# Kernel tuning notes

Hardware: AMD Instinct MI355X
Metric: run time of the kernel (lower is better)

The kernel has to match this reference:

```python
import jax, jax.numpy as jnp
import numpy as np

B, N, D, H, QK, HID = 4, 1024, 1024, 16, 64, 4096
BETA = 1.0 / float(np.sqrt(QK))  # default attn_beta = 1/sqrt(qk_dim)


def setup_inputs() -> dict:
    key = jax.random.key(0)
    k1, k2, k3, k4 = jax.random.split(key, 4)
    x = jax.random.normal(k1, (B, N, D), dtype=jnp.float32)
    scale = 1.0 / float(np.sqrt(D))
    Wq = jax.random.normal(k2, (H, QK, D), dtype=jnp.float32) * scale
    Wk = jax.random.normal(k3, (H, QK, D), dtype=jnp.float32) * scale
    W_hop = jax.random.normal(k4, (D, HID), dtype=jnp.float32) * scale
    return {"x": x, "Wq": Wq, "Wk": Wk, "W_hop": W_hop}


def _energy(x, Wq, Wk, W_hop):
    # Graph energy attention (dense path, no adjacency / mask)
    q = jnp.einsum('bnd,hqd->bhnq', x, Wq)  # [B,H,N,QK]
    k = jnp.einsum('bnd,hqd->bhnq', x, Wk)  # [B,H,N,QK]
    scores = BETA * jnp.einsum('bhnq,bhmq->bhnm', q, k)  # [B,H,N,N]
    e_attn = -(1.0 / BETA) * jnp.sum(jax.nn.logsumexp(scores, axis=-1))
    # Hopfield energy: -1/2 * sum relu(x W)^2
    h = jax.nn.relu(jnp.einsum('bnd,de->bne', x, W_hop))  # [B,N,HID]
    e_hop = -0.5 * jnp.sum(h * h)
    return e_attn + e_hop


def reference(x, Wq, Wk, W_hop):
    # Module returns (grad of energy w.r.t. x, energy) via grad_and_value
    energy, grad = jax.value_and_grad(_energy, argnums=0)(x, Wq, Wk, W_hop)
    return grad, energy
```

## Files before the change

kernel.cpp:

```cpp
#include <hip/hip_runtime.h>
#include <hip/hip_bf16.h>
#include <math.h>

#define BETA 0.125f
#define INV_BETA 8.0f

typedef __attribute__((ext_vector_type(8))) short short8v;
typedef __attribute__((ext_vector_type(4))) float f32x4;
typedef union { short8v v; unsigned short u[8]; } v8u;

#define OFF_XB   0u
#define OFF_WCB  2097152u
#define OFF_WCTB 3145728u
#define OFF_WHB  4194304u
#define OFF_WHTB 6291456u
#define OFF_H    8388608u
#define OFF_QB   16777216u
#define OFF_KB   18874368u
#define OFF_QT   20971520u
#define OFF_KT   23068672u
#define OFF_DQK  25165824u
#define OFF_LSE  29360128u
#define OFF_PL   29425664u
#define OFF_PH   29427712u

__device__ __forceinline__ unsigned short f2b(float f) {
    unsigned u = __float_as_uint(f);
    return (unsigned short)((u + 0x7fffu + ((u >> 16) & 1u)) >> 16);
}

__device__ __forceinline__ void gload_lds16(const unsigned short* g, void* l) {
    __builtin_amdgcn_global_load_lds(
        (const __attribute__((address_space(1))) unsigned int*)g,
        (__attribute__((address_space(3))) unsigned int*)l, 16, 0, 0);
}

__global__ __launch_bounds__(256) void k_cast(const float* __restrict__ src,
                                              unsigned short* __restrict__ dst, int n4) {
    int i = blockIdx.x * 256 + threadIdx.x;
    if (i < n4) {
        float4 v = ((const float4*)src)[i];
        ushort4 o;
        o.x = f2b(v.x); o.y = f2b(v.y); o.z = f2b(v.z); o.w = f2b(v.w);
        ((ushort4*)dst)[i] = o;
    }
}

__global__ void k_tcatb(const float* __restrict__ Wq, const float* __restrict__ Wk,
                        unsigned short* __restrict__ WCTB) {
    __shared__ float t[32][33];
    int j0 = blockIdx.x * 32, d0 = blockIdx.y * 32;
    int tx = threadIdx.x, ty = threadIdx.y;
#pragma unroll
    for (int i = 0; i < 4; ++i) {
        int j = j0 + ty + 8 * i;
        const float* src = (j < 1024) ? (Wq + (size_t)j * 1024) : (Wk + (size_t)(j - 1024) * 1024);
        t[ty + 8 * i][tx] = src[d0 + tx];
    }
    __syncthreads();
#pragma unroll
    for (int i = 0; i < 4; ++i)
        WCTB[(size_t)(d0 + ty + 8 * i) * 2048 + j0 + tx] = f2b(t[tx][ty + 8 * i]);
}

__global__ void k_thopb(const float* __restrict__ Whop, unsigned short* __restrict__ WHTB) {
    __shared__ float t[32][33];
    int e0 = blockIdx.x * 32, d0 = blockIdx.y * 32;
    int tx = threadIdx.x, ty = threadIdx.y;
#pragma unroll
    for (int i = 0; i < 4; ++i)
        t[ty + 8 * i][tx] = Whop[(size_t)(d0 + ty + 8 * i) * 4096 + e0 + tx];
    __syncthreads();
#pragma unroll
    for (int i = 0; i < 4; ++i)
        WHTB[(size_t)(e0 + ty + 8 * i) * 1024 + d0 + tx] = f2b(t[tx][ty + 8 * i]);
}

template <int NJ>
__device__ __forceinline__ void gemm_core(const unsigned short* __restrict__ A, int lda,
                                          const unsigned short* __restrict__ Bm, int ldb,
                                          int kdim, int rowBase, int colBase,
                                          unsigned short* ldsA, unsigned short* ldsB,
                                          f32x4 (&acc)[4][NJ]) {
    const int tid = threadIdx.x, lane = tid & 63;
    const int wv = tid >> 6;
    const int lr = lane & 15, lg = lane >> 4;
    const int wrow = (wv >> 1) * 64;
    const int wcol = (wv & 1) * (NJ * 16);

    for (int kk = 0; kk < kdim; kk += 64) {
#pragma unroll
        for (int iss = 0; iss < 4; ++iss) {
            int p = iss * 256 + tid;
            int row = p >> 3, c = p & 7, cs = c ^ (row & 7);
            gload_lds16(&A[(size_t)(rowBase + row) * lda + kk + cs * 8], (char*)ldsA + p * 16);
        }
#pragma unroll
        for (int iss = 0; iss < NJ; ++iss) {
            int p = iss * 256 + tid;
            int row = p >> 3, c = p & 7, cs = c ^ (row & 7);
            gload_lds16(&Bm[(size_t)(colBase + row) * ldb + kk + cs * 8], (char*)ldsB + p * 16);
        }
        __syncthreads();
#pragma unroll
        for (int kc = 0; kc < 2; ++kc) {
            short8v av[4], bv[NJ];
#pragma unroll
            for (int i = 0; i < 4; ++i) {
                int row = wrow + i * 16 + lr;
                int phys = row * 128 + ((kc * 4 + lg) ^ (row & 7)) * 16;
                av[i] = *(const short8v*)((const char*)ldsA + phys);
            }
#pragma unroll
            for (int j = 0; j < NJ; ++j) {
                int row = wcol + j * 16 + lr;
                int phys = row * 128 + ((kc * 4 + lg) ^ (row & 7)) * 16;
                bv[j] = *(const short8v*)((const char*)ldsB + phys);
            }
#pragma unroll
            for (int i = 0; i < 4; ++i)
#pragma unroll
                for (int j = 0; j < NJ; ++j)
                    acc[i][j] = __builtin_amdgcn_mfma_f32_16x16x32_bf16(av[i], bv[j], acc[i][j], 0, 0, 0);
        }
        __syncthreads();
    }
}

#define GEMM_SETUP(NJ)                                                           \
    __shared__ unsigned short ldsA[128 * 64];                                    \
    __shared__ unsigned short ldsB[NJ * 32 * 64];                                \
    const int tid = threadIdx.x, lane = tid & 63, wv = tid >> 6;                 \
    const int lr = lane & 15, lg = lane >> 4;                                    \
    const int row0 = blockIdx.x * 128 + (wv >> 1) * 64;                          \
    const int col0 = blockIdx.y * (NJ * 32) + (wv & 1) * (NJ * 16);              \
    f32x4 acc[4][NJ];                                                            \
    _Pragma("unroll") for (int i = 0; i < 4; ++i)                                \
        _Pragma("unroll") for (int j = 0; j < NJ; ++j)                           \
            acc[i][j] = (f32x4){0.f, 0.f, 0.f, 0.f};

__global__ __launch_bounds__(256) void mm_proj(const unsigned short* __restrict__ XB,
                                               const unsigned short* __restrict__ WCB,
                                               unsigned short* __restrict__ Qb,
                                               unsigned short* __restrict__ Kb) {
    GEMM_SETUP(4)
    gemm_core<4>(XB, 1024, WCB, 1024, 1024, blockIdx.x * 128, blockIdx.y * 128, ldsA, ldsB, acc);
    unsigned short* dst = (col0 < 1024) ? Qb : Kb;
    const int cbase = col0 & 1023;
#pragma unroll
    for (int i = 0; i < 4; ++i)
#pragma unroll
        for (int r = 0; r < 4; ++r) {
            int rg = row0 + i * 16 + lg * 4 + r;
            int bb = rg >> 10, n = rg & 1023;
#pragma unroll
            for (int j = 0; j < 4; ++j) {
                int c = cbase + j * 16 + lr;
                int h = c >> 6, q = c & 63;
                dst[((size_t)(bb * 16 + h) * 1024 + n) * 64 + q] = f2b(acc[i][j][r]);
            }
        }
}

__global__ __launch_bounds__(256) void mm_hopfwd(const unsigned short* __restrict__ XB,
                                                 const unsigned short* __restrict__ WHTB,
                                                 unsigned short* __restrict__ H,
                                                 float* __restrict__ PH) {
    __shared__ float red[4];
    GEMM_SETUP(4)
    gemm_core<4>(XB, 1024, WHTB, 1024, 1024, blockIdx.x * 128, blockIdx.y * 128, ldsA, ldsB, acc);
    float ss = 0.f;
#pragma unroll
    for (int i = 0; i < 4; ++i)
#pragma unroll
        for (int r = 0; r < 4; ++r) {
            size_t rg = row0 + i * 16 + lg * 4 + r;
#pragma unroll
            for (int j = 0; j < 4; ++j) {
                float hv = fmaxf(acc[i][j][r], 0.f);
                ss += hv * hv;
                H[rg * 4096 + col0 + j * 16 + lr] = f2b(hv);
            }
        }
#pragma unroll
    for (int off = 32; off; off >>= 1) ss += __shfl_down(ss, off);
    if (lane == 0) red[wv] = ss;
    __syncthreads();
    if (tid == 0) PH[blockIdx.y * gridDim.x + blockIdx.x] = red[0] + red[1] + red[2] + red[3];
}

__global__ __launch_bounds__(256) void mm_hopbwd(const unsigned short* __restrict__ H,
                                                 const unsigned short* __restrict__ WHB,
                                                 float* __restrict__ out) {
    GEMM_SETUP(2)
    gemm_core<2>(H, 4096, WHB, 4096, 4096, blockIdx.x * 128, blockIdx.y * 64, ldsA, ldsB, acc);
#pragma unroll
    for (int i = 0; i < 4; ++i)
#pragma unroll
        for (int r = 0; r < 4; ++r) {
            size_t rg = row0 + i * 16 + lg * 4 + r;
#pragma unroll
            for (int j = 0; j < 2; ++j)
                out[rg * 1024 + col0 + j * 16 + lr] = -acc[i][j][r];
        }
}

__global__ __launch_bounds__(256) void mm_gradproj(const unsigned short* __restrict__ DQK,
                                                   const unsigned short* __restrict__ WCTB,
                                                   float* __restrict__ out) {
    GEMM_SETUP(2)
    gemm_core<2>(DQK, 2048, WCTB, 2048, 2048, blockIdx.x * 128, blockIdx.y * 64, ldsA, ldsB, acc);
#pragma unroll
    for (int i = 0; i < 4; ++i)
#pragma unroll
        for (int r = 0; r < 4; ++r) {
            size_t rg = row0 + i * 16 + lg * 4 + r;
#pragma unroll
            for (int j = 0; j < 2; ++j) {
                size_t idx = rg * 1024 + col0 + j * 16 + lr;
                out[idx] += acc[i][j][r];
            }
        }
}

__global__ __launch_bounds__(256) void k_tqk(const unsigned short* __restrict__ Qb,
                                             const unsigned short* __restrict__ Kb,
                                             unsigned short* __restrict__ QT,
                                             unsigned short* __restrict__ KT) {
    __shared__ unsigned short T[64][65];
    const int z = blockIdx.z;
    const unsigned short* src = z ? Kb : Qb;
    unsigned short* dst = z ? KT : QT;
    const int bh = blockIdx.y;
    const int n0 = blockIdx.x * 64;
    const int t = threadIdx.x;
    {
        int row = t >> 3;
        int colc = (t & 7) * 8;
#pragma unroll
        for (int ii = 0; ii < 2; ++ii) {
            int r = row + 32 * ii;
            v8u vv;
            vv.v = *(const short8v*)&src[((size_t)(bh << 10) + n0 + r) * 64 + colc];
#pragma unroll
            for (int j = 0; j < 8; ++j) T[r][colc + j] = vv.u[j];
        }
    }
    __syncthreads();
    {
        int q = t >> 2;
        int nc = (t & 3) * 16;
        unsigned short buf[16];
#pragma unroll
        for (int j = 0; j < 16; ++j) buf[j] = T[nc + j][q];
        *(short8v*)&dst[((size_t)bh * 64 + q) * 1024 + n0 + nc] = *(short8v*)&buf[0];
        *(short8v*)&dst[((size_t)bh * 64 + q) * 1024 + n0 + nc + 8] = *(short8v*)&buf[8];
    }
}

__global__ __launch_bounds__(256) void k_dq(const unsigned short* __restrict__ Qb,
                                            const unsigned short* __restrict__ Kb,
                                            const unsigned short* __restrict__ KT,
                                            float* __restrict__ LSE,
                                            float* __restrict__ PL,
                                            unsigned short* __restrict__ DQK) {
    __shared__ unsigned short Ktile[2][64 * 64];
    __shared__ unsigned short Ttile[2][64 * 64];
    __shared__ unsigned short P[4][2048];
    const int tid = threadIdx.x, lane = tid & 63, wv = tid >> 6;
    const int bh = blockIdx.x, nt = blockIdx.y;
    const int nw = nt * 128 + wv * 32;
    const int lr = lane & 15, lg = lane >> 4;
    unsigned short* Pw = &P[wv][0];

    auto stage = [&](int buf, int m0) {
#pragma unroll
        for (int iss = 0; iss < 2; ++iss) {
            int p = iss * 256 + tid;
            int row = p >> 3, c = p & 7, cs = c ^ (row & 7);
            gload_lds16(&Kb[((size_t)(bh << 10) + m0 + row) * 64 + cs * 8],
                        (char*)&Ktile[buf][0] + p * 16);
            gload_lds16(&KT[((size_t)bh * 64 + row) * 1024 + m0 + cs * 8],
                        (char*)&Ttile[buf][0] + p * 16);
        }
    };

    short8v qa[2][2];
#pragma unroll
    for (int rb = 0; rb < 2; ++rb)
#pragma unroll
        for (int kc = 0; kc < 2; ++kc)
            qa[rb][kc] = *(const short8v*)&Qb[((size_t)(bh << 10) + nw + rb * 16 + lr) * 64 + kc * 32 + lg * 8];

    float sm[2][4];
    f32x4 dq[2][4];
#pragma unroll
    for (int rb = 0; rb < 2; ++rb) {
#pragma unroll
        for (int r = 0; r < 4; ++r) sm[rb][r] = 0.f;
#pragma unroll
        for (int qb = 0; qb < 4; ++qb) dq[rb][qb] = (f32x4){0.f, 0.f, 0.f, 0.f};
    }

    stage(0, 0);
    __syncthreads();
    int buf = 0;
    for (int mt = 0; mt < 16; ++mt) {
        if (mt < 15) stage(buf ^ 1, (mt + 1) * 64);
        const char* Kt = (const char*)&Ktile[buf][0];
        const char* Tt = (const char*)&Ttile[buf][0];
#pragma unroll
        for (int ct = 0; ct < 4; ++ct) {
            int brow = ct * 16 + lr;
            short8v bk0 = *(const short8v*)(Kt + brow * 128 + ((lg) ^ (brow & 7)) * 16);
            short8v bk1 = *(const short8v*)(Kt + brow * 128 + ((lg + 4) ^ (brow & 7)) * 16);
#pragma unroll
            for (int rb = 0; rb < 2; ++rb) {
                f32x4 s = {0.f, 0.f, 0.f, 0.f};
                s = __builtin_amdgcn_mfma_f32_16x16x32_bf16(qa[rb][0], bk0, s, 0, 0, 0);
                s = __builtin_amdgcn_mfma_f32_16x16x32_bf16(qa[rb][1], bk1, s, 0, 0, 0);
#pragma unroll
                for (int r = 0; r < 4; ++r) {
                    float p = __expf(s[r] * BETA);
                    sm[rb][r] += p;
                    int row = rb * 16 + lg * 4 + r;
                    int off = (row * 64 + ct * 16 + lr) ^ ((row & 7) << 3);
                    Pw[off] = f2b(p);
                }
            }
        }
        short8v pa[2][2];
#pragma unroll
        for (int rb = 0; rb < 2; ++rb) {
            int row = rb * 16 + lr;
#pragma unroll
            for (int kc = 0; kc < 2; ++kc) {
                int off = (row * 64 + kc * 32 + lg * 8) ^ ((row & 7) << 3);
                pa[rb][kc] = *(const short8v*)&Pw[off];
            }
        }
#pragma unroll
        for (int qb = 0; qb < 4; ++qb) {
            int brow = qb * 16 + lr;
            short8v b0 = *(const short8v*)(Tt + brow * 128 + ((lg) ^ (brow & 7)) * 16);
            short8v b1 = *(const short8v*)(Tt + brow * 128 + ((lg + 4) ^ (brow & 7)) * 16);
#pragma unroll
            for (int rb = 0; rb < 2; ++rb) {
                dq[rb][qb] = __builtin_amdgcn_mfma_f32_16x16x32_bf16(pa[rb][0], b0, dq[rb][qb], 0, 0, 0);
                dq[rb][qb] = __builtin_amdgcn_mfma_f32_16x16x32_bf16(pa[rb][1], b1, dq[rb][qb], 0, 0, 0);
            }
        }
        __syncthreads();
        buf ^= 1;
    }

#pragma unroll
    for (int off = 1; off < 16; off <<= 1)
#pragma unroll
        for (int rb = 0; rb < 2; ++rb)
#pragma unroll
            for (int r = 0; r < 4; ++r) sm[rb][r] += __shfl_xor(sm[rb][r], off);

    const int b = bh >> 4, h = bh & 15;
#pragma unroll
    for (int rb = 0; rb < 2; ++rb) {
#pragma unroll
        for (int r = 0; r < 4; ++r) {
            float inv = 1.0f / sm[rb][r];
#pragma unroll
            for (int qb = 0; qb < 4; ++qb)
                DQK[((size_t)(b << 10) + nw + rb * 16 + lg * 4 + r) * 2048 + h * 64 + qb * 16 + lr] =
                    f2b(-dq[rb][qb][r] * inv);
        }
    }

    float lsum = 0.f;
    if (lr == 0) {
#pragma unroll
        for (int rb = 0; rb < 2; ++rb)
#pragma unroll
            for (int r = 0; r < 4; ++r) {
                float l = __logf(sm[rb][r]);
                LSE[(size_t)(bh << 10) + nw + rb * 16 + lg * 4 + r] = l;
                lsum += l;
            }
    }
    lsum += __shfl_xor(lsum, 16);
    lsum += __shfl_xor(lsum, 32);
    if (lane == 0) PL[(size_t)(bh * 8 + nt) * 4 + wv] = lsum;
}

__global__ __launch_bounds__(256) void k_dk(const unsigned short* __restrict__ Qb,
                                            const unsigned short* __restrict__ Kb,
                                            const unsigned short* __restrict__ QT,
                                            const float* __restrict__ LSE,
                                            unsigned short* __restrict__ DQK) {
    __shared__ unsigned short Qtile[2][64 * 64];
    __shared__ unsigned short Ttile[2][64 * 64];
    __shared__ unsigned short P[4][2048];
    const int tid = threadIdx.x, lane = tid & 63, wv = tid >> 6;
    const int bh = blockIdx.x, mt = blockIdx.y;
    const int mw = mt * 128 + wv * 32;
    const int lr = lane & 15, lg = lane >> 4;
    unsigned short* Pw = &P[wv][0];

    auto stage = [&](int buf, int n0) {
#pragma unroll
        for (int iss = 0; iss < 2; ++iss) {
            int p = iss * 256 + tid;
            int row = p >> 3, c = p & 7, cs = c ^ (row & 7);
            gload_lds16(&Qb[((size_t)(bh << 10) + n0 + row) * 64 + cs * 8],
                        (char*)&Qtile[buf][0] + p * 16);
            gload_lds16(&QT[((size_t)bh * 64 + row) * 1024 + n0 + cs * 8],
                        (char*)&Ttile[buf][0] + p * 16);
        }
    };

    short8v ka[2][2];
#pragma unroll
    for (int rb = 0; rb < 2; ++rb)
#pragma unroll
        for (int kc = 0; kc < 2; ++kc)
            ka[rb][kc] = *(const short8v*)&Kb[((size_t)(bh << 10) + mw + rb * 16 + lr) * 64 + kc * 32 + lg * 8];

    f32x4 dk[2][4];
#pragma unroll
    for (int rb = 0; rb < 2; ++rb)
#pragma unroll
        for (int qb = 0; qb < 4; ++qb) dk[rb][qb] = (f32x4){0.f, 0.f, 0.f, 0.f};

    stage(0, 0);
    __syncthreads();
    int buf = 0;
    for (int ntl = 0; ntl < 16; ++ntl) {
        const int n0 = ntl * 64;
        float lse_c[4];
#pragma unroll
        for (int ct = 0; ct < 4; ++ct)
            lse_c[ct] = LSE[(size_t)(bh << 10) + n0 + ct * 16 + lr];
        if (ntl < 15) stage(buf ^ 1, n0 + 64);
        const char* Qt = (const char*)&Qtile[buf][0];
        const char* Tt = (const char*)&Ttile[buf][0];
#pragma unroll
        for (int ct = 0; ct < 4; ++ct) {
            int brow = ct * 16 + lr;
            short8v bq0 = *(const short8v*)(Qt + brow * 128 + ((lg) ^ (brow & 7)) * 16);
            short8v bq1 = *(const short8v*)(Qt + brow * 128 + ((lg + 4) ^ (brow & 7)) * 16);
#pragma unroll
            for (int rb = 0; rb < 2; ++rb) {
                f32x4 s = {0.f, 0.f, 0.f, 0.f};
                s = __builtin_amdgcn_mfma_f32_16x16x32_bf16(ka[rb][0], bq0, s, 0, 0, 0);
                s = __builtin_amdgcn_mfma_f32_16x16x32_bf16(ka[rb][1], bq1, s, 0, 0, 0);
#pragma unroll
                for (int r = 0; r < 4; ++r) {
                    float p = __expf(s[r] * BETA - lse_c[ct]);
                    int row = rb * 16 + lg * 4 + r;
                    int off = (row * 64 + ct * 16 + lr) ^ ((row & 7) << 3);
                    Pw[off] = f2b(p);
                }
            }
        }
        short8v pa[2][2];
#pragma unroll
        for (int rb = 0; rb < 2; ++rb) {
            int row = rb * 16 + lr;
#pragma unroll
            for (int kc = 0; kc < 2; ++kc) {
                int off = (row * 64 + kc * 32 + lg * 8) ^ ((row & 7) << 3);
                pa[rb][kc] = *(const short8v*)&Pw[off];
            }
        }
#pragma unroll
        for (int qb = 0; qb < 4; ++qb) {
            int brow = qb * 16 + lr;
            short8v b0 = *(const short8v*)(Tt + brow * 128 + ((lg) ^ (brow & 7)) * 16);
            short8v b1 = *(const short8v*)(Tt + brow * 128 + ((lg + 4) ^ (brow & 7)) * 16);
#pragma unroll
            for (int rb = 0; rb < 2; ++rb) {
                dk[rb][qb] = __builtin_amdgcn_mfma_f32_16x16x32_bf16(pa[rb][0], b0, dk[rb][qb], 0, 0, 0);
                dk[rb][qb] = __builtin_amdgcn_mfma_f32_16x16x32_bf16(pa[rb][1], b1, dk[rb][qb], 0, 0, 0);
            }
        }
        __syncthreads();
        buf ^= 1;
    }
    const int b = bh >> 4, h = bh & 15;
#pragma unroll
    for (int rb = 0; rb < 2; ++rb)
#pragma unroll
        for (int qb = 0; qb < 4; ++qb)
#pragma unroll
            for (int r = 0; r < 4; ++r)
                DQK[((size_t)(b << 10) + mw + rb * 16 + lg * 4 + r) * 2048 + 1024 + h * 64 + qb * 16 + lr] = f2b(-dk[rb][qb][r]);
}

__global__ __launch_bounds__(256) void k_fin(const float* __restrict__ pl,
                                             const float* __restrict__ ph,
                                             float* __restrict__ out) {
    const int tid = threadIdx.x;
    float s1 = 0.f, s2 = 0.f;
    for (int i = tid; i < 2048; i += 256) s1 += pl[i];
    for (int i = tid; i < 1024; i += 256) s2 += ph[i];
#pragma unroll
    for (int off = 32; off; off >>= 1) {
        s1 += __shfl_down(s1, off);
        s2 += __shfl_down(s2, off);
    }
    __shared__ float r1[4], r2[4];
    if ((tid & 63) == 0) { r1[tid >> 6] = s1; r2[tid >> 6] = s2; }
    __syncthreads();
    if (tid == 0) {
        float S1 = r1[0] + r1[1] + r1[2] + r1[3];
        float S2 = r2[0] + r2[1] + r2[2] + r2[3];
        out[(size_t)4194304] = -INV_BETA * S1 - 0.5f * S2;
    }
}

extern "C" void kernel_launch(void* const* d_in, const int* in_sizes, int n_in,
                              void* d_out, int out_size, void* d_ws, size_t ws_size,
                              hipStream_t stream) {
    (void)in_sizes; (void)n_in; (void)out_size; (void)ws_size;
    const float* x    = (const float*)d_in[0];
    const float* Wq   = (const float*)d_in[1];
    const float* Wk   = (const float*)d_in[2];
    const float* Whop = (const float*)d_in[3];
    float* out = (float*)d_out;
    float* ws = (float*)d_ws;

    unsigned short* XB   = (unsigned short*)(ws + OFF_XB);
    unsigned short* WCB  = (unsigned short*)(ws + OFF_WCB);
    unsigned short* WCTB = (unsigned short*)(ws + OFF_WCTB);
    unsigned short* WHB  = (unsigned short*)(ws + OFF_WHB);
    unsigned short* WHTB = (unsigned short*)(ws + OFF_WHTB);
    unsigned short* H    = (unsigned short*)(ws + OFF_H);
    unsigned short* Qb   = (unsigned short*)(ws + OFF_QB);
    unsigned short* Kb   = (unsigned short*)(ws + OFF_KB);
    unsigned short* QT   = (unsigned short*)(ws + OFF_QT);
    unsigned short* KT   = (unsigned short*)(ws + OFF_KT);
    unsigned short* DQK  = (unsigned short*)(ws + OFF_DQK);
    float* LSE = ws + OFF_LSE;
    float* PL  = ws + OFF_PL;
    float* PH  = ws + OFF_PH;

    dim3 blk(256);
    k_cast<<<dim3(4096), blk, 0, stream>>>(x, XB, 1048576);
    k_cast<<<dim3(1024), blk, 0, stream>>>(Wq, WCB, 262144);
    k_cast<<<dim3(1024), blk, 0, stream>>>(Wk, WCB + 1048576, 262144);
    k_cast<<<dim3(4096), blk, 0, stream>>>(Whop, WHB, 1048576);
    k_tcatb<<<dim3(64, 32), dim3(32, 8), 0, stream>>>(Wq, Wk, WCTB);
    k_thopb<<<dim3(128, 32), dim3(32, 8), 0, stream>>>(Whop, WHTB);

    mm_proj<<<dim3(32, 16), blk, 0, stream>>>(XB, WCB, Qb, Kb);
    k_tqk<<<dim3(16, 64, 2), blk, 0, stream>>>(Qb, Kb, QT, KT);
    k_dq<<<dim3(64, 8), blk, 0, stream>>>(Qb, Kb, KT, LSE, PL, DQK);
    k_dk<<<dim3(64, 8), blk, 0, stream>>>(Qb, Kb, QT, LSE, DQK);

    mm_hopfwd<<<dim3(32, 32), blk, 0, stream>>>(XB, WHTB, H, PH);
    mm_hopbwd<<<dim3(32, 16), blk, 0, stream>>>(H, WHB, out);
    mm_gradproj<<<dim3(32, 16), blk, 0, stream>>>(DQK, WCTB, out);
    k_fin<<<dim3(1), blk, 0, stream>>>(PL, PH, out);
}
```

Before: 328.0 us.

## Double-buffer LDS in GEMM cores and merge cast/transpose launches

Adds a double-buffered GEMM core that prefetches the next K tile into a second LDS buffer while MFMAs run on the current one, and uses it for the projection, Hopfield backward and gradient-projection GEMMs. The four cast kernels are merged into one launch, and the two transpose kernels into one, to cut launch overhead. Double buffering doubles LDS use per block, which may lower occupancy.

```diff
diff --git a/kernel.cpp b/kernel.cpp
--- a/kernel.cpp
+++ b/kernel.cpp
@@ -35,45 +35,55 @@
         (__attribute__((address_space(3))) unsigned int*)l, 16, 0, 0);
 }
 
-__global__ __launch_bounds__(256) void k_cast(const float* __restrict__ src,
-                                              unsigned short* __restrict__ dst, int n4) {
+__global__ __launch_bounds__(256) void k_castall(const float* __restrict__ x,
+                                                 const float* __restrict__ Wq,
+                                                 const float* __restrict__ Wk,
+                                                 const float* __restrict__ Whop,
+                                                 unsigned short* __restrict__ XB,
+                                                 unsigned short* __restrict__ WCB,
+                                                 unsigned short* __restrict__ WHB) {
     int i = blockIdx.x * 256 + threadIdx.x;
-    if (i < n4) {
-        float4 v = ((const float4*)src)[i];
-        ushort4 o;
-        o.x = f2b(v.x); o.y = f2b(v.y); o.z = f2b(v.z); o.w = f2b(v.w);
-        ((ushort4*)dst)[i] = o;
-    }
-}
-
-__global__ void k_tcatb(const float* __restrict__ Wq, const float* __restrict__ Wk,
-                        unsigned short* __restrict__ WCTB) {
+    const float* s;
+    unsigned short* d;
+    int j;
+    if (i < 1048576) { s = x; d = XB; j = i; }
+    else if (i < 1310720) { s = Wq; d = WCB; j = i - 1048576; }
+    else if (i < 1572864) { s = Wk; d = WCB + 1048576; j = i - 1310720; }
+    else { s = Whop; d = WHB; j = i - 1572864; }
+    float4 v = ((const float4*)s)[j];
+    ushort4 o;
+    o.x = f2b(v.x); o.y = f2b(v.y); o.z = f2b(v.z); o.w = f2b(v.w);
+    ((ushort4*)d)[j] = o;
+}
+
+__global__ void k_tall(const float* __restrict__ Wq, const float* __restrict__ Wk,
+                       const float* __restrict__ Whop,
+                       unsigned short* __restrict__ WCTB, unsigned short* __restrict__ WHTB) {
     __shared__ float t[32][33];
-    int j0 = blockIdx.x * 32, d0 = blockIdx.y * 32;
+    int bx = blockIdx.x;
     int tx = threadIdx.x, ty = threadIdx.y;
-#pragma unroll
-    for (int i = 0; i < 4; ++i) {
-        int j = j0 + ty + 8 * i;
-        const float* src = (j < 1024) ? (Wq + (size_t)j * 1024) : (Wk + (size_t)(j - 1024) * 1024);
-        t[ty + 8 * i][tx] = src[d0 + tx];
-    }
-    __syncthreads();
-#pragma unroll
-    for (int i = 0; i < 4; ++i)
-        WCTB[(size_t)(d0 + ty + 8 * i) * 2048 + j0 + tx] = f2b(t[tx][ty + 8 * i]);
-}
-
-__global__ void k_thopb(const float* __restrict__ Whop, unsigned short* __restrict__ WHTB) {
-    __shared__ float t[32][33];
-    int e0 = blockIdx.x * 32, d0 = blockIdx.y * 32;
-    int tx = threadIdx.x, ty = threadIdx.y;
-#pragma unroll
-    for (int i = 0; i < 4; ++i)
-        t[ty + 8 * i][tx] = Whop[(size_t)(d0 + ty + 8 * i) * 4096 + e0 + tx];
-    __syncthreads();
-#pragma unroll
-    for (int i = 0; i < 4; ++i)
-        WHTB[(size_t)(e0 + ty + 8 * i) * 1024 + d0 + tx] = f2b(t[tx][ty + 8 * i]);
+    if (bx < 64) {
+        int j0 = bx * 32, d0 = blockIdx.y * 32;
+#pragma unroll
+        for (int i = 0; i < 4; ++i) {
+            int j = j0 + ty + 8 * i;
+            const float* src = (j < 1024) ? (Wq + (size_t)j * 1024) : (Wk + (size_t)(j - 1024) * 1024);
+            t[ty + 8 * i][tx] = src[d0 + tx];
+        }
+        __syncthreads();
+#pragma unroll
+        for (int i = 0; i < 4; ++i)
+            WCTB[(size_t)(d0 + ty + 8 * i) * 2048 + j0 + tx] = f2b(t[tx][ty + 8 * i]);
+    } else {
+        int e0 = (bx - 64) * 32, d0 = blockIdx.y * 32;
+#pragma unroll
+        for (int i = 0; i < 4; ++i)
+            t[ty + 8 * i][tx] = Whop[(size_t)(d0 + ty + 8 * i) * 4096 + e0 + tx];
+        __syncthreads();
+#pragma unroll
+        for (int i = 0; i < 4; ++i)
+            WHTB[(size_t)(e0 + ty + 8 * i) * 1024 + d0 + tx] = f2b(t[tx][ty + 8 * i]);
+    }
 }
 
 template <int NJ>
@@ -127,9 +137,66 @@
     }
 }
 
-#define GEMM_SETUP(NJ)                                                           \
-    __shared__ unsigned short ldsA[128 * 64];                                    \
-    __shared__ unsigned short ldsB[NJ * 32 * 64];                                \
+template <int NJ>
+__device__ __forceinline__ void gemm_core_db(const unsigned short* __restrict__ A, int lda,
+                                             const unsigned short* __restrict__ Bm, int ldb,
+                                             int kdim, int rowBase, int colBase,
+                                             unsigned short (*ldsA)[128 * 64],
+                                             unsigned short (*ldsB)[NJ * 32 * 64],
+                                             f32x4 (&acc)[4][NJ]) {
+    const int tid = threadIdx.x, lane = tid & 63;
+    const int wv = tid >> 6;
+    const int lr = lane & 15, lg = lane >> 4;
+    const int wrow = (wv >> 1) * 64;
+    const int wcol = (wv & 1) * (NJ * 16);
+
+    auto stage = [&](int buf, int kk) {
+#pragma unroll
+        for (int iss = 0; iss < 4; ++iss) {
+            int p = iss * 256 + tid;
+            int row = p >> 3, c = p & 7, cs = c ^ (row & 7);
+            gload_lds16(&A[(size_t)(rowBase + row) * lda + kk + cs * 8], (char*)&ldsA[buf][0] + p * 16);
+        }
+#pragma unroll
+        for (int iss = 0; iss < NJ; ++iss) {
+            int p = iss * 256 + tid;
+            int row = p >> 3, c = p & 7, cs = c ^ (row & 7);
+            gload_lds16(&Bm[(size_t)(colBase + row) * ldb + kk + cs * 8], (char*)&ldsB[buf][0] + p * 16);
+        }
+    };
+
+    stage(0, 0);
+    __syncthreads();
+    int buf = 0;
+    for (int kk = 0; kk < kdim; kk += 64) {
+        if (kk + 64 < kdim) stage(buf ^ 1, kk + 64);
+        const char* La = (const char*)&ldsA[buf][0];
+        const char* Lb = (const char*)&ldsB[buf][0];
+#pragma unroll
+        for (int kc = 0; kc < 2; ++kc) {
+            short8v av[4], bv[NJ];
+#pragma unroll
+            for (int i = 0; i < 4; ++i) {
+                int row = wrow + i * 16 + lr;
+                av[i] = *(const short8v*)(La + row * 128 + ((kc * 4 + lg) ^ (row & 7)) * 16);
+            }
+#pragma unroll
+            for (int j = 0; j < NJ; ++j) {
+                int row = wcol + j * 16 + lr;
+                bv[j] = *(const short8v*)(Lb + row * 128 + ((kc * 4 + lg) ^ (row & 7)) * 16);
+            }
+#pragma unroll
+            for (int i = 0; i < 4; ++i)
+#pragma unroll
+                for (int j = 0; j < NJ; ++j)
+                    acc[i][j] = __builtin_amdgcn_mfma_f32_16x16x32_bf16(av[i], bv[j], acc[i][j], 0, 0, 0);
+        }
+        __syncthreads();
+        buf ^= 1;
+    }
+}
+
+#define GEMM_IDX(NJ)                                                             \
     const int tid = threadIdx.x, lane = tid & 63, wv = tid >> 6;                 \
     const int lr = lane & 15, lg = lane >> 4;                                    \
     const int row0 = blockIdx.x * 128 + (wv >> 1) * 64;                          \
@@ -143,8 +210,10 @@
                                                const unsigned short* __restrict__ WCB,
                                                unsigned short* __restrict__ Qb,
                                                unsigned short* __restrict__ Kb) {
-    GEMM_SETUP(4)
-    gemm_core<4>(XB, 1024, WCB, 1024, 1024, blockIdx.x * 128, blockIdx.y * 128, ldsA, ldsB, acc);
+    __shared__ unsigned short ldsA[2][128 * 64];
+    __shared__ unsigned short ldsB[2][128 * 64];
+    GEMM_IDX(4)
+    gemm_core_db<4>(XB, 1024, WCB, 1024, 1024, blockIdx.x * 128, blockIdx.y * 128, ldsA, ldsB, acc);
     unsigned short* dst = (col0 < 1024) ? Qb : Kb;
     const int cbase = col0 & 1023;
 #pragma unroll
@@ -166,8 +235,10 @@
                                                  const unsigned short* __restrict__ WHTB,
                                                  unsigned short* __restrict__ H,
                                                  float* __restrict__ PH) {
+    __shared__ unsigned short ldsA[128 * 64];
+    __shared__ unsigned short ldsB[128 * 64];
     __shared__ float red[4];
-    GEMM_SETUP(4)
+    GEMM_IDX(4)
     gemm_core<4>(XB, 1024, WHTB, 1024, 1024, blockIdx.x * 128, blockIdx.y * 128, ldsA, ldsB, acc);
     float ss = 0.f;
 #pragma unroll
@@ -192,8 +263,10 @@
 __global__ __launch_bounds__(256) void mm_hopbwd(const unsigned short* __restrict__ H,
                                                  const unsigned short* __restrict__ WHB,
                                                  float* __restrict__ out) {
-    GEMM_SETUP(2)
-    gemm_core<2>(H, 4096, WHB, 4096, 4096, blockIdx.x * 128, blockIdx.y * 64, ldsA, ldsB, acc);
+    __shared__ unsigned short ldsA[2][128 * 64];
+    __shared__ unsigned short ldsB[2][64 * 64];
+    GEMM_IDX(2)
+    gemm_core_db<2>(H, 4096, WHB, 4096, 4096, blockIdx.x * 128, blockIdx.y * 64, ldsA, ldsB, acc);
 #pragma unroll
     for (int i = 0; i < 4; ++i)
 #pragma unroll
@@ -208,8 +281,10 @@
 __global__ __launch_bounds__(256) void mm_gradproj(const unsigned short* __restrict__ DQK,
                                                    const unsigned short* __restrict__ WCTB,
                                                    float* __restrict__ out) {
-    GEMM_SETUP(2)
-    gemm_core<2>(DQK, 2048, WCTB, 2048, 2048, blockIdx.x * 128, blockIdx.y * 64, ldsA, ldsB, acc);
+    __shared__ unsigned short ldsA[2][128 * 64];
+    __shared__ unsigned short ldsB[2][64 * 64];
+    GEMM_IDX(2)
+    gemm_core_db<2>(DQK, 2048, WCTB, 2048, 2048, blockIdx.x * 128, blockIdx.y * 64, ldsA, ldsB, acc);
 #pragma unroll
     for (int i = 0; i < 4; ++i)
 #pragma unroll
@@ -543,12 +618,8 @@
     float* PH  = ws + OFF_PH;
 
     dim3 blk(256);
-    k_cast<<<dim3(4096), blk, 0, stream>>>(x, XB, 1048576);
-    k_cast<<<dim3(1024), blk, 0, stream>>>(Wq, WCB, 262144);
-    k_cast<<<dim3(1024), blk, 0, stream>>>(Wk, WCB + 1048576, 262144);
-    k_cast<<<dim3(4096), blk, 0, stream>>>(Whop, WHB, 1048576);
-    k_tcatb<<<dim3(64, 32), dim3(32, 8), 0, stream>>>(Wq, Wk, WCTB);
-    k_thopb<<<dim3(128, 32), dim3(32, 8), 0, stream>>>(Whop, WHTB);
+    k_castall<<<dim3(10240), blk, 0, stream>>>(x, Wq, Wk, Whop, XB, WCB, WHB);
+    k_tall<<<dim3(192, 32), dim3(32, 8), 0, stream>>>(Wq, Wk, Whop, WCTB, WHTB);
 
     mm_proj<<<dim3(32, 16), blk, 0, stream>>>(XB, WCB, Qb, Kb);
     k_tqk<<<dim3(16, 64, 2), blk, 0, stream>>>(Qb, Kb, QT, KT);
```

New measurement: 329.2 us. About the same (+0.4%).

## Shrink GEMM and attention tiles for more blocks; merge cast/transpose launches

Applied to the files above, without the earlier changes.

Templates the GEMM core on the row-tile count and halves the row tile for the projection, hop-backward and grad-projection GEMMs. This doubles their grid to 1024 blocks on a 256-CU device. The dq/dk attention kernels drop from 32 rows per wave to 16, which doubles their block count, and the partial-LSE buffer and final reduction grow to match. The six cast/transpose launches are merged into two kernels to cut launch overhead. The cost is less data reuse per block and more total loads of the shared operands.

```diff
diff --git a/kernel.cpp b/kernel.cpp
--- a/kernel.cpp
+++ b/kernel.cpp
@@ -22,7 +22,7 @@
 #define OFF_DQK  25165824u
 #define OFF_LSE  29360128u
 #define OFF_PL   29425664u
-#define OFF_PH   29427712u
+#define OFF_PH   29429760u
 
 __device__ __forceinline__ unsigned short f2b(float f) {
     unsigned u = __float_as_uint(f);
@@ -35,62 +35,72 @@
         (__attribute__((address_space(3))) unsigned int*)l, 16, 0, 0);
 }
 
-__global__ __launch_bounds__(256) void k_cast(const float* __restrict__ src,
-                                              unsigned short* __restrict__ dst, int n4) {
+__global__ __launch_bounds__(256) void k_castall(const float* __restrict__ x,
+                                                 const float* __restrict__ Wq,
+                                                 const float* __restrict__ Wk,
+                                                 const float* __restrict__ Whop,
+                                                 unsigned short* __restrict__ XB,
+                                                 unsigned short* __restrict__ WCB,
+                                                 unsigned short* __restrict__ WHB) {
     int i = blockIdx.x * 256 + threadIdx.x;
-    if (i < n4) {
-        float4 v = ((const float4*)src)[i];
-        ushort4 o;
-        o.x = f2b(v.x); o.y = f2b(v.y); o.z = f2b(v.z); o.w = f2b(v.w);
-        ((ushort4*)dst)[i] = o;
-    }
-}
-
-__global__ void k_tcatb(const float* __restrict__ Wq, const float* __restrict__ Wk,
-                        unsigned short* __restrict__ WCTB) {
+    const float* s;
+    unsigned short* d;
+    int j;
+    if (i < 1048576) { s = x; d = XB; j = i; }
+    else if (i < 1310720) { s = Wq; d = WCB; j = i - 1048576; }
+    else if (i < 1572864) { s = Wk; d = WCB + 1048576; j = i - 1310720; }
+    else { s = Whop; d = WHB; j = i - 1572864; }
+    float4 v = ((const float4*)s)[j];
+    ushort4 o;
+    o.x = f2b(v.x); o.y = f2b(v.y); o.z = f2b(v.z); o.w = f2b(v.w);
+    ((ushort4*)d)[j] = o;
+}
+
+__global__ void k_tall(const float* __restrict__ Wq, const float* __restrict__ Wk,
+                       const float* __restrict__ Whop,
+                       unsigned short* __restrict__ WCTB, unsigned short* __restrict__ WHTB) {
     __shared__ float t[32][33];
-    int j0 = blockIdx.x * 32, d0 = blockIdx.y * 32;
+    int bx = blockIdx.x;
     int tx = threadIdx.x, ty = threadIdx.y;
-#pragma unroll
-    for (int i = 0; i < 4; ++i) {
-        int j = j0 + ty + 8 * i;
-        const float* src = (j < 1024) ? (Wq + (size_t)j * 1024) : (Wk + (size_t)(j - 1024) * 1024);
-        t[ty + 8 * i][tx] = src[d0 + tx];
-    }
-    __syncthreads();
-#pragma unroll
-    for (int i = 0; i < 4; ++i)
-        WCTB[(size_t)(d0 + ty + 8 * i) * 2048 + j0 + tx] = f2b(t[tx][ty + 8 * i]);
-}
-
-__global__ void k_thopb(const float* __restrict__ Whop, unsigned short* __restrict__ WHTB) {
-    __shared__ float t[32][33];
-    int e0 = blockIdx.x * 32, d0 = blockIdx.y * 32;
-    int tx = threadIdx.x, ty = threadIdx.y;
-#pragma unroll
-    for (int i = 0; i < 4; ++i)
-        t[ty + 8 * i][tx] = Whop[(size_t)(d0 + ty + 8 * i) * 4096 + e0 + tx];
-    __syncthreads();
-#pragma unroll
-    for (int i = 0; i < 4; ++i)
-        WHTB[(size_t)(e0 + ty + 8 * i) * 1024 + d0 + tx] = f2b(t[tx][ty + 8 * i]);
-}
-
-template <int NJ>
+    if (bx < 64) {
+        int j0 = bx * 32, d0 = blockIdx.y * 32;
+#pragma unroll
+        for (int i = 0; i < 4; ++i) {
+            int j = j0 + ty + 8 * i;
+            const float* src = (j < 1024) ? (Wq + (size_t)j * 1024) : (Wk + (size_t)(j - 1024) * 1024);
+            t[ty + 8 * i][tx] = src[d0 + tx];
+        }
+        __syncthreads();
+#pragma unroll
+        for (int i = 0; i < 4; ++i)
+            WCTB[(size_t)(d0 + ty + 8 * i) * 2048 + j0 + tx] = f2b(t[tx][ty + 8 * i]);
+    } else {
+        int e0 = (bx - 64) * 32, d0 = blockIdx.y * 32;
+#pragma unroll
+        for (int i = 0; i < 4; ++i)
+            t[ty + 8 * i][tx] = Whop[(size_t)(d0 + ty + 8 * i) * 4096 + e0 + tx];
+        __syncthreads();
+#pragma unroll
+        for (int i = 0; i < 4; ++i)
+            WHTB[(size_t)(e0 + ty + 8 * i) * 1024 + d0 + tx] = f2b(t[tx][ty + 8 * i]);
+    }
+}
+
+template <int MI, int NJ>
 __device__ __forceinline__ void gemm_core(const unsigned short* __restrict__ A, int lda,
                                           const unsigned short* __restrict__ Bm, int ldb,
                                           int kdim, int rowBase, int colBase,
                                           unsigned short* ldsA, unsigned short* ldsB,
-                                          f32x4 (&acc)[4][NJ]) {
+                                          f32x4 (&acc)[MI][NJ]) {
     const int tid = threadIdx.x, lane = tid & 63;
     const int wv = tid >> 6;
     const int lr = lane & 15, lg = lane >> 4;
-    const int wrow = (wv >> 1) * 64;
+    const int wrow = (wv >> 1) * (MI * 16);
     const int wcol = (wv & 1) * (NJ * 16);
 
     for (int kk = 0; kk < kdim; kk += 64) {
 #pragma unroll
-        for (int iss = 0; iss < 4; ++iss) {
+        for (int iss = 0; iss < MI; ++iss) {
             int p = iss * 256 + tid;
             int row = p >> 3, c = p & 7, cs = c ^ (row & 7);
             gload_lds16(&A[(size_t)(rowBase + row) * lda + kk + cs * 8], (char*)ldsA + p * 16);
@@ -104,21 +114,19 @@
         __syncthreads();
 #pragma unroll
         for (int kc = 0; kc < 2; ++kc) {
-            short8v av[4], bv[NJ];
-#pragma unroll
-            for (int i = 0; i < 4; ++i) {
+            short8v av[MI], bv[NJ];
+#pragma unroll
+            for (int i = 0; i < MI; ++i) {
                 int row = wrow + i * 16 + lr;
-                int phys = row * 128 + ((kc * 4 + lg) ^ (row & 7)) * 16;
-                av[i] = *(const short8v*)((const char*)ldsA + phys);
+                av[i] = *(const short8v*)((const char*)ldsA + row * 128 + ((kc * 4 + lg) ^ (row & 7)) * 16);
             }
 #pragma unroll
             for (int j = 0; j < NJ; ++j) {
                 int row = wcol + j * 16 + lr;
-                int phys = row * 128 + ((kc * 4 + lg) ^ (row & 7)) * 16;
-                bv[j] = *(const short8v*)((const char*)ldsB + phys);
-            }
-#pragma unroll
-            for (int i = 0; i < 4; ++i)
+                bv[j] = *(const short8v*)((const char*)ldsB + row * 128 + ((kc * 4 + lg) ^ (row & 7)) * 16);
+            }
+#pragma unroll
+            for (int i = 0; i < MI; ++i)
 #pragma unroll
                 for (int j = 0; j < NJ; ++j)
                     acc[i][j] = __builtin_amdgcn_mfma_f32_16x16x32_bf16(av[i], bv[j], acc[i][j], 0, 0, 0);
@@ -127,15 +135,13 @@
     }
 }
 
-#define GEMM_SETUP(NJ)                                                           \
-    __shared__ unsigned short ldsA[128 * 64];                                    \
-    __shared__ unsigned short ldsB[NJ * 32 * 64];                                \
+#define GEMM_IDX(MI, NJ)                                                         \
     const int tid = threadIdx.x, lane = tid & 63, wv = tid >> 6;                 \
     const int lr = lane & 15, lg = lane >> 4;                                    \
-    const int row0 = blockIdx.x * 128 + (wv >> 1) * 64;                          \
+    const int row0 = blockIdx.x * (MI * 32) + (wv >> 1) * (MI * 16);             \
     const int col0 = blockIdx.y * (NJ * 32) + (wv & 1) * (NJ * 16);              \
-    f32x4 acc[4][NJ];                                                            \
-    _Pragma("unroll") for (int i = 0; i < 4; ++i)                                \
+    f32x4 acc[MI][NJ];                                                           \
+    _Pragma("unroll") for (int i = 0; i < MI; ++i)                               \
         _Pragma("unroll") for (int j = 0; j < NJ; ++j)                           \
             acc[i][j] = (f32x4){0.f, 0.f, 0.f, 0.f};
 
@@ -143,12 +149,14 @@
                                                const unsigned short* __restrict__ WCB,
                                                unsigned short* __restrict__ Qb,
                                                unsigned short* __restrict__ Kb) {
-    GEMM_SETUP(4)
-    gemm_core<4>(XB, 1024, WCB, 1024, 1024, blockIdx.x * 128, blockIdx.y * 128, ldsA, ldsB, acc);
+    __shared__ unsigned short ldsA[64 * 64];
+    __shared__ unsigned short ldsB[128 * 64];
+    GEMM_IDX(2, 4)
+    gemm_core<2, 4>(XB, 1024, WCB, 1024, 1024, blockIdx.x * 64, blockIdx.y * 128, ldsA, ldsB, acc);
     unsigned short* dst = (col0 < 1024) ? Qb : Kb;
     const int cbase = col0 & 1023;
 #pragma unroll
-    for (int i = 0; i < 4; ++i)
+    for (int i = 0; i < 2; ++i)
 #pragma unroll
         for (int r = 0; r < 4; ++r) {
             int rg = row0 + i * 16 + lg * 4 + r;
@@ -166,9 +174,11 @@
                                                  const unsigned short* __restrict__ WHTB,
                                                  unsigned short* __restrict__ H,
                                                  float* __restrict__ PH) {
+    __shared__ unsigned short ldsA[128 * 64];
+    __shared__ unsigned short ldsB[128 * 64];
     __shared__ float red[4];
-    GEMM_SETUP(4)
-    gemm_core<4>(XB, 1024, WHTB, 1024, 1024, blockIdx.x * 128, blockIdx.y * 128, ldsA, ldsB, acc);
+    GEMM_IDX(4, 4)
+    gemm_core<4, 4>(XB, 1024, WHTB, 1024, 1024, blockIdx.x * 128, blockIdx.y * 128, ldsA, ldsB, acc);
     float ss = 0.f;
 #pragma unroll
     for (int i = 0; i < 4; ++i)
@@ -192,10 +202,12 @@
 __global__ __launch_bounds__(256) void mm_hopbwd(const unsigned short* __restrict__ H,
                                                  const unsigned short* __restrict__ WHB,
                                                  float* __restrict__ out) {
-    GEMM_SETUP(2)
-    gemm_core<2>(H, 4096, WHB, 4096, 4096, blockIdx.x * 128, blockIdx.y * 64, ldsA, ldsB, acc);
-#pragma unroll
-    for (int i = 0; i < 4; ++i)
+    __shared__ unsigned short ldsA[64 * 64];
+    __shared__ unsigned short ldsB[64 * 64];
+    GEMM_IDX(2, 2)
+    gemm_core<2, 2>(H, 4096, WHB, 4096, 4096, blockIdx.x * 64, blockIdx.y * 64, ldsA, ldsB, acc);
+#pragma unroll
+    for (int i = 0; i < 2; ++i)
 #pragma unroll
         for (int r = 0; r < 4; ++r) {
             size_t rg = row0 + i * 16 + lg * 4 + r;
@@ -208,10 +220,12 @@
 __global__ __launch_bounds__(256) void mm_gradproj(const unsigned short* __restrict__ DQK,
                                                    const unsigned short* __restrict__ WCTB,
                                                    float* __restrict__ out) {
-    GEMM_SETUP(2)
-    gemm_core<2>(DQK, 2048, WCTB, 2048, 2048, blockIdx.x * 128, blockIdx.y * 64, ldsA, ldsB, acc);
-#pragma unroll
-    for (int i = 0; i < 4; ++i)
+    __shared__ unsigned short ldsA[64 * 64];
+    __shared__ unsigned short ldsB[64 * 64];
+    GEMM_IDX(2, 2)
+    gemm_core<2, 2>(DQK, 2048, WCTB, 2048, 2048, blockIdx.x * 64, blockIdx.y * 64, ldsA, ldsB, acc);
+#pragma unroll
+    for (int i = 0; i < 2; ++i)
 #pragma unroll
         for (int r = 0; r < 4; ++r) {
             size_t rg = row0 + i * 16 + lg * 4 + r;
@@ -266,10 +280,10 @@
                                             unsigned short* __restrict__ DQK) {
     __shared__ unsigned short Ktile[2][64 * 64];
     __shared__ unsigned short Ttile[2][64 * 64];
-    __shared__ unsigned short P[4][2048];
+    __shared__ unsigned short P[4][1024];
     const int tid = threadIdx.x, lane = tid & 63, wv = tid >> 6;
     const int bh = blockIdx.x, nt = blockIdx.y;
-    const int nw = nt * 128 + wv * 32;
+    const int nw = nt * 64 + wv * 16;
     const int lr = lane & 15, lg = lane >> 4;
     unsigned short* Pw = &P[wv][0];
 
@@ -285,22 +299,17 @@
         }
     };
 
-    short8v qa[2][2];
-#pragma unroll
-    for (int rb = 0; rb < 2; ++rb)
-#pragma unroll
-        for (int kc = 0; kc < 2; ++kc)
-            qa[rb][kc] = *(const short8v*)&Qb[((size_t)(bh << 10) + nw + rb * 16 + lr) * 64 + kc * 32 + lg * 8];
-
-    float sm[2][4];
-    f32x4 dq[2][4];
-#pragma unroll
-    for (int rb = 0; rb < 2; ++rb) {
-#pragma unroll
-        for (int r = 0; r < 4; ++r) sm[rb][r] = 0.f;
-#pragma unroll
-        for (int qb = 0; qb < 4; ++qb) dq[rb][qb] = (f32x4){0.f, 0.f, 0.f, 0.f};
-    }
+    short8v qa[2];
+#pragma unroll
+    for (int kc = 0; kc < 2; ++kc)
+        qa[kc] = *(const short8v*)&Qb[((size_t)(bh << 10) + nw + lr) * 64 + kc * 32 + lg * 8];
+
+    float sm[4];
+    f32x4 dq[4];
+#pragma unroll
+    for (int r = 0; r < 4; ++r) sm[r] = 0.f;
+#pragma unroll
+    for (int qb = 0; qb < 4; ++qb) dq[qb] = (f32x4){0.f, 0.f, 0.f, 0.f};
 
     stage(0, 0);
     __syncthreads();
@@ -314,41 +323,31 @@
             int brow = ct * 16 + lr;
             short8v bk0 = *(const short8v*)(Kt + brow * 128 + ((lg) ^ (brow & 7)) * 16);
             short8v bk1 = *(const short8v*)(Kt + brow * 128 + ((lg + 4) ^ (brow & 7)) * 16);
-#pragma unroll
-            for (int rb = 0; rb < 2; ++rb) {
-                f32x4 s = {0.f, 0.f, 0.f, 0.f};
-                s = __builtin_amdgcn_mfma_f32_16x16x32_bf16(qa[rb][0], bk0, s, 0, 0, 0);
-                s = __builtin_amdgcn_mfma_f32_16x16x32_bf16(qa[rb][1], bk1, s, 0, 0, 0);
-#pragma unroll
-                for (int r = 0; r < 4; ++r) {
-                    float p = __expf(s[r] * BETA);
-                    sm[rb][r] += p;
-                    int row = rb * 16 + lg * 4 + r;
-                    int off = (row * 64 + ct * 16 + lr) ^ ((row & 7) << 3);
-                    Pw[off] = f2b(p);
-                }
-            }
-        }
-        short8v pa[2][2];
-#pragma unroll
-        for (int rb = 0; rb < 2; ++rb) {
-            int row = rb * 16 + lr;
-#pragma unroll
-            for (int kc = 0; kc < 2; ++kc) {
-                int off = (row * 64 + kc * 32 + lg * 8) ^ ((row & 7) << 3);
-                pa[rb][kc] = *(const short8v*)&Pw[off];
-            }
+            f32x4 s = {0.f, 0.f, 0.f, 0.f};
+            s = __builtin_amdgcn_mfma_f32_16x16x32_bf16(qa[0], bk0, s, 0, 0, 0);
+            s = __builtin_amdgcn_mfma_f32_16x16x32_bf16(qa[1], bk1, s, 0, 0, 0);
+#pragma unroll
+            for (int r = 0; r < 4; ++r) {
+                float p = __expf(s[r] * BETA);
+                sm[r] += p;
+                int row = lg * 4 + r;
+                int off = (row * 64 + ct * 16 + lr) ^ ((row & 7) << 3);
+                Pw[off] = f2b(p);
+            }
+        }
+        short8v pa[2];
+#pragma unroll
+        for (int kc = 0; kc < 2; ++kc) {
+            int off = (lr * 64 + kc * 32 + lg * 8) ^ ((lr & 7) << 3);
+            pa[kc] = *(const short8v*)&Pw[off];
         }
 #pragma unroll
         for (int qb = 0; qb < 4; ++qb) {
             int brow = qb * 16 + lr;
             short8v b0 = *(const short8v*)(Tt + brow * 128 + ((lg) ^ (brow & 7)) * 16);
             short8v b1 = *(const short8v*)(Tt + brow * 128 + ((lg + 4) ^ (brow & 7)) * 16);
-#pragma unroll
-            for (int rb = 0; rb < 2; ++rb) {
-                dq[rb][qb] = __builtin_amdgcn_mfma_f32_16x16x32_bf16(pa[rb][0], b0, dq[rb][qb], 0, 0, 0);
-                dq[rb][qb] = __builtin_amdgcn_mfma_f32_16x16x32_bf16(pa[rb][1], b1, dq[rb][qb], 0, 0, 0);
-            }
+            dq[qb] = __builtin_amdgcn_mfma_f32_16x16x32_bf16(pa[0], b0, dq[qb], 0, 0, 0);
+            dq[qb] = __builtin_amdgcn_mfma_f32_16x16x32_bf16(pa[1], b1, dq[qb], 0, 0, 0);
         }
         __syncthreads();
         buf ^= 1;
@@ -357,37 +356,30 @@
 #pragma unroll
     for (int off = 1; off < 16; off <<= 1)
 #pragma unroll
-        for (int rb = 0; rb < 2; ++rb)
-#pragma unroll
-            for (int r = 0; r < 4; ++r) sm[rb][r] += __shfl_xor(sm[rb][r], off);
+        for (int r = 0; r < 4; ++r) sm[r] += __shfl_xor(sm[r], off);
 
     const int b = bh >> 4, h = bh & 15;
 #pragma unroll
-    for (int rb = 0; rb < 2; ++rb) {
-#pragma unroll
-        for (int r = 0; r < 4; ++r) {
-            float inv = 1.0f / sm[rb][r];
-#pragma unroll
-            for (int qb = 0; qb < 4; ++qb)
-                DQK[((size_t)(b << 10) + nw + rb * 16 + lg * 4 + r) * 2048 + h * 64 + qb * 16 + lr] =
-                    f2b(-dq[rb][qb][r] * inv);
-        }
+    for (int r = 0; r < 4; ++r) {
+        float inv = 1.0f / sm[r];
+#pragma unroll
+        for (int qb = 0; qb < 4; ++qb)
+            DQK[((size_t)(b << 10) + nw + lg * 4 + r) * 2048 + h * 64 + qb * 16 + lr] =
+                f2b(-dq[qb][r] * inv);
     }
 
     float lsum = 0.f;
     if (lr == 0) {
 #pragma unroll
-        for (int rb = 0; rb < 2; ++rb)
-#pragma unroll
-            for (int r = 0; r < 4; ++r) {
-                float l = __logf(sm[rb][r]);
-                LSE[(size_t)(bh << 10) + nw + rb * 16 + lg * 4 + r] = l;
-                lsum += l;
-            }
+        for (int r = 0; r < 4; ++r) {
+            float l = __logf(sm[r]);
+            LSE[(size_t)(bh << 10) + nw + lg * 4 + r] = l;
+            lsum += l;
+        }
     }
     lsum += __shfl_xor(lsum, 16);
     lsum += __shfl_xor(lsum, 32);
-    if (lane == 0) PL[(size_t)(bh * 8 + nt) * 4 + wv] = lsum;
+    if (lane == 0) PL[(size_t)(bh * 16 + nt) * 4 + wv] = lsum;
 }
 
 __global__ __launch_bounds__(256) void k_dk(const unsigned short* __restrict__ Qb,
@@ -397,10 +389,10 @@
                                             unsigned short* __restrict__ DQK) {
     __shared__ unsigned short Qtile[2][64 * 64];
     __shared__ unsigned short Ttile[2][64 * 64];
-    __shared__ unsigned short P[4][2048];
+    __shared__ unsigned short P[4][1024];
     const int tid = threadIdx.x, lane = tid & 63, wv = tid >> 6;
     const int bh = blockIdx.x, mt = blockIdx.y;
-    const int mw = mt * 128 + wv * 32;
+    const int mw = mt * 64 + wv * 16;
     const int lr = lane & 15, lg = lane >> 4;
     unsigned short* Pw = &P[wv][0];
 
@@ -416,18 +408,14 @@
         }
     };
 
-    short8v ka[2][2];
-#pragma unroll
-    for (int rb = 0; rb < 2; ++rb)
-#pragma unroll
-        for (int kc = 0; kc < 2; ++kc)
-            ka[rb][kc] = *(const short8v*)&Kb[((size_t)(bh << 10) + mw + rb * 16 + lr) * 64 + kc * 32 + lg * 8];
-
-    f32x4 dk[2][4];
-#pragma unroll
-    for (int rb = 0; rb < 2; ++rb)
-#pragma unroll
-        for (int qb = 0; qb < 4; ++qb) dk[rb][qb] = (f32x4){0.f, 0.f, 0.f, 0.f};
+    short8v ka[2];
+#pragma unroll
+    for (int kc = 0; kc < 2; ++kc)
+        ka[kc] = *(const short8v*)&Kb[((size_t)(bh << 10) + mw + lr) * 64 + kc * 32 + lg * 8];
+
+    f32x4 dk[4];
+#pragma unroll
+    for (int qb = 0; qb < 4; ++qb) dk[qb] = (f32x4){0.f, 0.f, 0.f, 0.f};
 
     stage(0, 0);
     __syncthreads();
@@ -446,52 +434,40 @@
             int brow = ct * 16 + lr;
             short8v bq0 = *(const short8v*)(Qt + brow * 128 + ((lg) ^ (brow & 7)) * 16);
             short8v bq1 = *(const short8v*)(Qt + brow * 128 + ((lg + 4) ^ (brow & 7)) * 16);
-#pragma unroll
-            for (int rb = 0; rb < 2; ++rb) {
-                f32x4 s = {0.f, 0.f, 0.f, 0.f};
-                s = __builtin_amdgcn_mfma_f32_16x16x32_bf16(ka[rb][0], bq0, s, 0, 0, 0);
-                s = __builtin_amdgcn_mfma_f32_16x16x32_bf16(ka[rb][1], bq1, s, 0, 0, 0);
-#pragma unroll
-                for (int r = 0; r < 4; ++r) {
-                    float p = __expf(s[r] * BETA - lse_c[ct]);
-                    int row = rb * 16 + lg * 4 + r;
-                    int off = (row * 64 + ct * 16 + lr) ^ ((row & 7) << 3);
-                    Pw[off] = f2b(p);
-                }
-            }
-        }
-        short8v pa[2][2];
-#pragma unroll
-        for (int rb = 0; rb < 2; ++rb) {
-            int row = rb * 16 + lr;
-#pragma unroll
-            for (int kc = 0; kc < 2; ++kc) {
-                int off = (row * 64 + kc * 32 + lg * 8) ^ ((row & 7) << 3);
-                pa[rb][kc] = *(const short8v*)&Pw[off];
-            }
+            f32x4 s = {0.f, 0.f, 0.f, 0.f};
+            s = __builtin_amdgcn_mfma_f32_16x16x32_bf16(ka[0], bq0, s, 0, 0, 0);
+            s = __builtin_amdgcn_mfma_f32_16x16x32_bf16(ka[1], bq1, s, 0, 0, 0);
+#pragma unroll
+            for (int r = 0; r < 4; ++r) {
+                float p = __expf(s[r] * BETA - lse_c[ct]);
+                int row = lg * 4 + r;
+                int off = (row * 64 + ct * 16 + lr) ^ ((row & 7) << 3);
+                Pw[off] = f2b(p);
+            }
+        }
+        short8v pa[2];
+#pragma unroll
+        for (int kc = 0; kc < 2; ++kc) {
+            int off = (lr * 64 + kc * 32 + lg * 8) ^ ((lr & 7) << 3);
+            pa[kc] = *(const short8v*)&Pw[off];
         }
 #pragma unroll
         for (int qb = 0; qb < 4; ++qb) {
             int brow = qb * 16 + lr;
             short8v b0 = *(const short8v*)(Tt + brow * 128 + ((lg) ^ (brow & 7)) * 16);
             short8v b1 = *(const short8v*)(Tt + brow * 128 + ((lg + 4) ^ (brow & 7)) * 16);
-#pragma unroll
-            for (int rb = 0; rb < 2; ++rb) {
-                dk[rb][qb] = __builtin_amdgcn_mfma_f32_16x16x32_bf16(pa[rb][0], b0, dk[rb][qb], 0, 0, 0);
-                dk[rb][qb] = __builtin_amdgcn_mfma_f32_16x16x32_bf16(pa[rb][1], b1, dk[rb][qb], 0, 0, 0);
-            }
+            dk[qb] = __builtin_amdgcn_mfma_f32_16x16x32_bf16(pa[0], b0, dk[qb], 0, 0, 0);
+            dk[qb] = __builtin_amdgcn_mfma_f32_16x16x32_bf16(pa[1], b1, dk[qb], 0, 0, 0);
         }
         __syncthreads();
         buf ^= 1;
     }
     const int b = bh >> 4, h = bh & 15;
 #pragma unroll
-    for (int rb = 0; rb < 2; ++rb)
-#pragma unroll
-        for (int qb = 0; qb < 4; ++qb)
-#pragma unroll
-            for (int r = 0; r < 4; ++r)
-                DQK[((size_t)(b << 10) + mw + rb * 16 + lg * 4 + r) * 2048 + 1024 + h * 64 + qb * 16 + lr] = f2b(-dk[rb][qb][r]);
+    for (int qb = 0; qb < 4; ++qb)
+#pragma unroll
+        for (int r = 0; r < 4; ++r)
+            DQK[((size_t)(b << 10) + mw + lg * 4 + r) * 2048 + 1024 + h * 64 + qb * 16 + lr] = f2b(-dk[qb][r]);
 }
 
 __global__ __launch_bounds__(256) void k_fin(const float* __restrict__ pl,
@@ -499,7 +475,7 @@
                                              float* __restrict__ out) {
     const int tid = threadIdx.x;
     float s1 = 0.f, s2 = 0.f;
-    for (int i = tid; i < 2048; i += 256) s1 += pl[i];
+    for (int i = tid; i < 4096; i += 256) s1 += pl[i];
     for (int i = tid; i < 1024; i += 256) s2 += ph[i];
 #pragma unroll
     for (int off = 32; off; off >>= 1) {
@@ -543,20 +519,16 @@
     float* PH  = ws + OFF_PH;
 
     dim3 blk(256);
-    k_cast<<<dim3(4096), blk, 0, stream>>>(x, XB, 1048576);
-    k_cast<<<dim3(1024), blk, 0, stream>>>(Wq, WCB, 262144);
-    k_cast<<<dim3(1024), blk, 0, stream>>>(Wk, WCB + 1048576, 262144);
-    k_cast<<<dim3(4096), blk, 0, stream>>>(Whop, WHB, 1048576);
-    k_tcatb<<<dim3(64, 32), dim3(32, 8), 0, stream>>>(Wq, Wk, WCTB);
-    k_thopb<<<dim3(128, 32), dim3(32, 8), 0, stream>>>(Whop, WHTB);
-
-    mm_proj<<<dim3(32, 16), blk, 0, stream>>>(XB, WCB, Qb, Kb);
+    k_castall<<<dim3(10240), blk, 0, stream>>>(x, Wq, Wk, Whop, XB, WCB, WHB);
+    k_tall<<<dim3(192, 32), dim3(32, 8), 0, stream>>>(Wq, Wk, Whop, WCTB, WHTB);
+
+    mm_proj<<<dim3(64, 16), blk, 0, stream>>>(XB, WCB, Qb, Kb);
     k_tqk<<<dim3(16, 64, 2), blk, 0, stream>>>(Qb, Kb, QT, KT);
-    k_dq<<<dim3(64, 8), blk, 0, stream>>>(Qb, Kb, KT, LSE, PL, DQK);
-    k_dk<<<dim3(64, 8), blk, 0, stream>>>(Qb, Kb, QT, LSE, DQK);
+    k_dq<<<dim3(64, 16), blk, 0, stream>>>(Qb, Kb, KT, LSE, PL, DQK);
+    k_dk<<<dim3(64, 16), blk, 0, stream>>>(Qb, Kb, QT, LSE, DQK);
 
     mm_hopfwd<<<dim3(32, 32), blk, 0, stream>>>(XB, WHTB, H, PH);
-    mm_hopbwd<<<dim3(32, 16), blk, 0, stream>>>(H, WHB, out);
-    mm_gradproj<<<dim3(32, 16), blk, 0, stream>>>(DQK, WCTB, out);
+    mm_hopbwd<<<dim3(64, 16), blk, 0, stream>>>(H, WHB, out);
+    mm_gradproj<<<dim3(64, 16), blk, 0, stream>>>(DQK, WCTB, out);
     k_fin<<<dim3(1), blk, 0, stream>>>(PL, PH, out);
 }
```

Measured after the change: 330.2 us. No clear change (+0.7%).
